# Performance work log

Measured on AMD Instinct MI355X. Metric: run time of the kernel, lower is better.

## Reference

```python
import jax, jax.numpy as jnp
import numpy as np

D_MODEL = 1024
DK = 64
H = D_MODEL // DK
EPS = 1e-5


def setup_inputs() -> dict:
    key = jax.random.key(0)
    ks = jax.random.split(key, 8)
    B, M = 4, 2048
    s = 1.0 / np.sqrt(D_MODEL)
    return {
        "inp": jax.random.normal(ks[0], (B, M, D_MODEL), dtype=jnp.float32),
        "Wq": jax.random.normal(ks[1], (D_MODEL, D_MODEL), dtype=jnp.float32) * s,
        "bq": jnp.zeros((D_MODEL,), dtype=jnp.float32),
        "Wk": jax.random.normal(ks[2], (D_MODEL, D_MODEL), dtype=jnp.float32) * s,
        "bk": jnp.zeros((D_MODEL,), dtype=jnp.float32),
        "Wv": jax.random.normal(ks[3], (D_MODEL, D_MODEL), dtype=jnp.float32) * s,
        "bv": jnp.zeros((D_MODEL,), dtype=jnp.float32),
        "gamma": jnp.ones((D_MODEL,), dtype=jnp.float32),
        "beta": jnp.zeros((D_MODEL,), dtype=jnp.float32),
    }


def reference(inp, Wq, bq, Wk, bk, Wv, bv, gamma, beta):
    B, M, _ = inp.shape
    # LayerNorm over last dim
    mu = jnp.mean(inp, axis=-1, keepdims=True)
    var = jnp.mean(jnp.square(inp - mu), axis=-1, keepdims=True)
    out = (inp - mu) * jax.lax.rsqrt(var + EPS) * gamma + beta
    # QKV projections (x @ W + b)
    Q = (out @ Wq + bq).reshape(B, M, DK, H)
    K = (out @ Wk + bk).reshape(B, M, DK, H)
    V = (out @ Wv + bv).reshape(B, M, DK, H)
    # per-position attention over the dk axis, contracting h
    scores = jnp.einsum("bmih,bmjh->bmij", Q, K) / np.sqrt(DK)  # [B,M,dk,dk]
    att = jax.nn.softmax(scores, axis=-1)
    res = jnp.einsum("bmij,bmjh->bmih", att, V).reshape(B, M, D_MODEL)
    # dropout is identity at eval; positionals add in original is dead code
    return inp + res
```

## Files before the change

### kernel.cpp

```cpp
#include <hip/hip_runtime.h>
#include <hip/hip_bf16.h>

#define D_MODEL 1024
#define NQKV 3072

typedef __attribute__((ext_vector_type(8))) short bf16x8;
typedef __attribute__((ext_vector_type(4))) float f32x4;
typedef __attribute__((ext_vector_type(16))) float f32x16;
typedef __attribute__((ext_vector_type(8))) unsigned short u16x8;

static __device__ __forceinline__ unsigned short f2bf(float f){
  unsigned int x = __float_as_uint(f);
  x += 0x7fff + ((x >> 16) & 1);
  return (unsigned short)(x >> 16);
}
static __device__ __forceinline__ float bf2f(unsigned short u){
  return __uint_as_float(((unsigned int)u) << 16);
}

__global__ __launch_bounds__(256) void ln_kernel(const float* __restrict__ inp,
    const float* __restrict__ gamma, const float* __restrict__ beta,
    unsigned short* __restrict__ X){
  const int row = blockIdx.x;
  const int t = threadIdx.x;
  const float4* ip = (const float4*)(inp + (size_t)row * D_MODEL);
  float4 v = ip[t];
  float s1 = v.x + v.y + v.z + v.w;
  float s2 = v.x*v.x + v.y*v.y + v.z*v.z + v.w*v.w;
#pragma unroll
  for (int off = 32; off >= 1; off >>= 1){
    s1 += __shfl_down(s1, off);
    s2 += __shfl_down(s2, off);
  }
  __shared__ float red[8];
  const int wave = t >> 6, lane = t & 63;
  if (lane == 0){ red[wave] = s1; red[4 + wave] = s2; }
  __syncthreads();
  s1 = red[0] + red[1] + red[2] + red[3];
  s2 = red[4] + red[5] + red[6] + red[7];
  const float mu   = s1 * (1.0f / D_MODEL);
  const float var  = s2 * (1.0f / D_MODEL) - mu * mu;
  const float rstd = rsqrtf(var + 1e-5f);
  float4 g = ((const float4*)gamma)[t];
  float4 b = ((const float4*)beta)[t];
  ushort4 o;
  o.x = f2bf((v.x - mu) * rstd * g.x + b.x);
  o.y = f2bf((v.y - mu) * rstd * g.y + b.y);
  o.z = f2bf((v.z - mu) * rstd * g.z + b.z);
  o.w = f2bf((v.w - mu) * rstd * g.w + b.w);
  ((ushort4*)(X + (size_t)row * D_MODEL))[t] = o;
}

__global__ __launch_bounds__(256) void wtrans_kernel(const float* __restrict__ Wq,
    const float* __restrict__ Wk, const float* __restrict__ Wv,
    const float* __restrict__ bq, const float* __restrict__ bk,
    const float* __restrict__ bv, unsigned short* __restrict__ Wt,
    float* __restrict__ bc){
  __shared__ float tile[32][33];
  const int z = blockIdx.z;
  const float* W = (z == 0) ? Wq : ((z == 1) ? Wk : Wv);
  const int k0 = blockIdx.x * 32, n0 = blockIdx.y * 32;
  const int r = threadIdx.x >> 5, c = threadIdx.x & 31;
  if (blockIdx.x == 0 && r == 0){
    const float* bsrc = (z == 0) ? bq : ((z == 1) ? bk : bv);
    bc[z * 1024 + n0 + c] = bsrc[n0 + c];
  }
#pragma unroll
  for (int i = 0; i < 4; i++)
    tile[r + i*8][c] = W[(size_t)(k0 + r + i*8) * D_MODEL + n0 + c];
  __syncthreads();
  unsigned short* dst = Wt + (size_t)(z * D_MODEL + n0) * D_MODEL + k0;
#pragma unroll
  for (int i = 0; i < 4; i++){
    int rr = r + i*8;
    dst[(size_t)rr * D_MODEL + c] = f2bf(tile[c][rr]);
  }
}


#define GLL(src, dst) __builtin_amdgcn_global_load_lds( \
    (const __attribute__((address_space(1))) void*)(src), \
    (__attribute__((address_space(3))) void*)(dst), 16, 0, 0)

#define STAGE(tsrc, bi) do { \
  _Pragma("unroll") \
  for (int q = 0; q < 4; q++){ \
    const int idx = q*512 + tid; \
    const int row = idx >> 3; \
    const size_t scol = (size_t)((tsrc)*128) + (((idx & 7)*16) ^ ((row & 7) << 4)); \
    GLL(Ag + (size_t)row*2048 + scol, ldsS + (size_t)(bi)*65536 + idx*16); \
    GLL(Bg + (size_t)row*2048 + scol, ldsS + (size_t)(bi)*65536 + 32768 + idx*16); \
  } \
} while(0)

#define BODY(bi) do { \
  const char* Ab = ldsS + (size_t)(bi)*65536 + (wr*128 + lr)*128; \
  const char* Bb = ldsS + (size_t)(bi)*65536 + 32768 + (wc*64 + lr)*128; \
  _Pragma("unroll") \
  for (int kh = 0; kh < 2; kh++){ \
    const int cb = kh ? colb1 : colb0; \
    bf16x8 Ar[8], Br[4]; \
    _Pragma("unroll") \
    for (int m = 0; m < 8; m++) Ar[m] = *(const bf16x8*)(Ab + m*2048 + cb); \
    _Pragma("unroll") \
    for (int n = 0; n < 4; n++) Br[n] = *(const bf16x8*)(Bb + n*2048 + cb); \
    _Pragma("unroll") \
    for (int m = 0; m < 8; m++) \
      _Pragma("unroll") \
      for (int n = 0; n < 4; n++) \
        acc[m][n] = __builtin_amdgcn_mfma_f32_16x16x32_bf16(Ar[m], Br[n], acc[m][n], 0, 0, 0); \
  } \
} while(0)

#define BARRIER __builtin_amdgcn_s_barrier()
#define SCHEDB  __builtin_amdgcn_sched_barrier(0)
#define VMCNT0  asm volatile("s_waitcnt vmcnt(0)" ::: "memory")

__global__ __launch_bounds__(512, 2) void gemm256_kernel(const unsigned short* __restrict__ A,
    const unsigned short* __restrict__ Bt, const float* __restrict__ bias,
    unsigned short* __restrict__ C){
  __shared__ __align__(16) char ldsS[2 * 65536];
  const int tid = threadIdx.x;
  const int wave = tid >> 6, lane = tid & 63;
  const int wr = wave >> 2, wc = wave & 3;
  const int lr = lane & 15;
  const int x7 = (lane & 7) << 4;
  const int colb0 = ((lane >> 4) * 16) ^ x7;
  const int colb1 = (64 + (lane >> 4) * 16) ^ x7;

  const int b = blockIdx.x;
  const int swz = (b & 7) * 48 + (b >> 3);
  const int m0 = (swz & 31) * 256;
  const int n0 = (swz >> 5) * 256;

  const char* Ag = (const char*)(A + (size_t)m0 * 1024);
  const char* Bg = (const char*)(Bt + (size_t)n0 * 1024);

  f32x4 acc[8][4] = {};

  STAGE(0, 0);
  SCHEDB; VMCNT0; BARRIER; SCHEDB;

  int buf = 0;
  for (int t = 0; t < 16; ++t, buf ^= 1){
    if (t < 15) STAGE(t + 1, buf ^ 1);
    BODY(buf);
    if (t < 15) { SCHEDB; VMCNT0; BARRIER; SCHEDB; }
  }

  const int gm = m0 + wr*128;
  const int gn = n0 + wc*64;
  const int rr0 = (lane >> 4) * 4;
#pragma unroll
  for (int nf = 0; nf < 4; nf++){
    const int gcol = gn + nf*16 + lr;
    const float bb = bias[gcol];
#pragma unroll
    for (int mf = 0; mf < 8; mf++){
      const int grow = gm + mf*16 + rr0;
#pragma unroll
      for (int r = 0; r < 4; r++)
        C[(size_t)(grow + r) * NQKV + gcol] = f2bf(acc[mf][nf][r] + bb);
    }
  }
}

__global__ __launch_bounds__(256) void attn_kernel(const unsigned short* __restrict__ qkv,
    const float* __restrict__ inp, float* __restrict__ out){
  __shared__ unsigned short P[4][64 * 64];
  const int wave = threadIdx.x >> 6, lane = threadIdx.x & 63;
  const int token = blockIdx.x * 4 + wave;
  const unsigned short* row = qkv + (size_t)token * NQKV;
  const int l31 = lane & 31, hi = lane >> 5;
  const int l15 = lane & 15, qg = lane >> 4;
  char* pbase = (char*)&P[wave][0];

  bf16x8 kf[2], qf[2];
#pragma unroll
  for (int mt = 0; mt < 2; mt++)
    kf[mt] = *(const bf16x8*)(row + 1024 + (mt*32 + l31)*16 + hi*8);
#pragma unroll
  for (int nt = 0; nt < 2; nt++)
    qf[nt] = *(const bf16x8*)(row + (nt*32 + l31)*16 + hi*8);

  bf16x8 vf[2];
#pragma unroll
  for (int kc = 0; kc < 2; kc++)
#pragma unroll
    for (int e = 0; e < 8; e++)
      vf[kc][e] = (short)row[2048 + (kc*32 + qg*8 + e)*16 + l15];

  f32x16 s[2][2] = {};
#pragma unroll
  for (int mt = 0; mt < 2; mt++)
#pragma unroll
    for (int nt = 0; nt < 2; nt++)
      s[mt][nt] = __builtin_amdgcn_mfma_f32_32x32x16_bf16(kf[mt], qf[nt], s[mt][nt], 0, 0, 0);

#pragma unroll
  for (int ti = 0; ti < 2; ti++){
    float m = s[0][ti][0];
#pragma unroll
    for (int mt = 0; mt < 2; mt++)
#pragma unroll
      for (int r = 0; r < 16; r++) m = fmaxf(m, s[mt][ti][r]);
    m = fmaxf(m, __shfl_xor(m, 32));
    float sum = 0.0f;
#pragma unroll
    for (int mt = 0; mt < 2; mt++)
#pragma unroll
      for (int r = 0; r < 16; r++){
        float p = exp2f((s[mt][ti][r] - m) * 0.1803368801f);
        s[mt][ti][r] = p;
        sum += p;
      }
    sum += __shfl_xor(sum, 32);
    const float invs = 1.0f / sum;
    const int i = ti*32 + l31;
    const int sw = (i & 7) << 4;
#pragma unroll
    for (int mt = 0; mt < 2; mt++)
#pragma unroll
      for (int g = 0; g < 4; g++){
        ushort4 pk;
        pk.x = f2bf(s[mt][ti][4*g + 0] * invs);
        pk.y = f2bf(s[mt][ti][4*g + 1] * invs);
        pk.z = f2bf(s[mt][ti][4*g + 2] * invs);
        pk.w = f2bf(s[mt][ti][4*g + 3] * invs);
        const int jbyte = mt*64 + g*16 + hi*8;
        *(ushort4*)(pbase + ((i*128 + jbyte) ^ sw)) = pk;
      }
  }
  __syncthreads();

  f32x4 o[4] = {};
#pragma unroll
  for (int nt = 0; nt < 4; nt++){
    const int n = nt*16 + l15;
    const int swr = (n & 7) << 4;
#pragma unroll
    for (int kc = 0; kc < 2; kc++){
      bf16x8 pb = *(const bf16x8*)(pbase + ((n*128 + kc*64 + qg*16) ^ swr));
      o[nt] = __builtin_amdgcn_mfma_f32_16x16x32_bf16(vf[kc], pb, o[nt], 0, 0, 0);
    }
  }

  const size_t base = (size_t)token * D_MODEL;
#pragma unroll
  for (int nt = 0; nt < 4; nt++){
    const int i = nt*16 + l15;
    const float4 iv = *(const float4*)(inp + base + i*16 + qg*4);
    float4 ov;
    ov.x = iv.x + o[nt][0];
    ov.y = iv.y + o[nt][1];
    ov.z = iv.z + o[nt][2];
    ov.w = iv.w + o[nt][3];
    *(float4*)(out + base + i*16 + qg*4) = ov;
  }
}

extern "C" void kernel_launch(void* const* d_in, const int* in_sizes, int n_in,
                              void* d_out, int out_size, void* d_ws, size_t ws_size,
                              hipStream_t stream) {
  const float* inp   = (const float*)d_in[0];
  const float* Wq    = (const float*)d_in[1];
  const float* bq    = (const float*)d_in[2];
  const float* Wk    = (const float*)d_in[3];
  const float* bk    = (const float*)d_in[4];
  const float* Wv    = (const float*)d_in[5];
  const float* bv    = (const float*)d_in[6];
  const float* gamma = (const float*)d_in[7];
  const float* beta  = (const float*)d_in[8];
  float* out = (float*)d_out;

  char* ws = (char*)d_ws;
  unsigned short* Xln  = (unsigned short*)ws;
  unsigned short* Wt   = (unsigned short*)(ws + 16777216);
  float*          bc   = (float*)(ws + 23068672);
  unsigned short* QKV  = (unsigned short*)(ws + 23080960);

  ln_kernel<<<8192, 256, 0, stream>>>(inp, gamma, beta, Xln);
  wtrans_kernel<<<dim3(32, 32, 3), 256, 0, stream>>>(Wq, Wk, Wv, bq, bk, bv, Wt, bc);
  gemm256_kernel<<<384, 512, 0, stream>>>(Xln, Wt, bc, QKV);
  attn_kernel<<<2048, 256, 0, stream>>>(QKV, inp, out);
}
```

Before: 105.1 us.

## Restructure QKV GEMM into per-wave private LDS staging with 128x256 tiles

```diff
diff --git a/kernel.cpp b/kernel.cpp
--- a/kernel.cpp
+++ b/kernel.cpp
@@ -82,81 +82,79 @@
     (const __attribute__((address_space(1))) void*)(src), \
     (__attribute__((address_space(3))) void*)(dst), 16, 0, 0)
 
-#define STAGE(tsrc, bi) do { \
-  _Pragma("unroll") \
-  for (int q = 0; q < 4; q++){ \
-    const int idx = q*512 + tid; \
-    const int row = idx >> 3; \
-    const size_t scol = (size_t)((tsrc)*128) + (((idx & 7)*16) ^ ((row & 7) << 4)); \
-    GLL(Ag + (size_t)row*2048 + scol, ldsS + (size_t)(bi)*65536 + idx*16); \
-    GLL(Bg + (size_t)row*2048 + scol, ldsS + (size_t)(bi)*65536 + 32768 + idx*16); \
+#define STG(t, bi) do { \
+  _Pragma("unroll") \
+  for (int j = 0; j < 4; j++){ \
+    GLL(As + (size_t)j*32768 + (size_t)(t)*64, dstL + (bi)*8192 + j*1024); \
+    GLL(Bs + (size_t)j*32768 + (size_t)(t)*64, dstL + (bi)*8192 + 4096 + j*1024); \
   } \
 } while(0)
 
-#define BODY(bi) do { \
-  const char* Ab = ldsS + (size_t)(bi)*65536 + (wr*128 + lr)*128; \
-  const char* Bb = ldsS + (size_t)(bi)*65536 + 32768 + (wc*64 + lr)*128; \
-  _Pragma("unroll") \
-  for (int kh = 0; kh < 2; kh++){ \
-    const int cb = kh ? colb1 : colb0; \
-    bf16x8 Ar[8], Br[4]; \
+#define BDY(bi) do { \
+  const char* Ab = wlds + (bi)*8192 + fo; \
+  const char* Bb = Ab + 4096; \
+  bf16x8 Af[4], Bf[4]; \
+  _Pragma("unroll") \
+  for (int m = 0; m < 4; m++) Af[m] = *(const bf16x8*)(Ab + m*1024); \
+  _Pragma("unroll") \
+  for (int n = 0; n < 4; n++) Bf[n] = *(const bf16x8*)(Bb + n*1024); \
+  _Pragma("unroll") \
+  for (int m = 0; m < 4; m++) \
     _Pragma("unroll") \
-    for (int m = 0; m < 8; m++) Ar[m] = *(const bf16x8*)(Ab + m*2048 + cb); \
-    _Pragma("unroll") \
-    for (int n = 0; n < 4; n++) Br[n] = *(const bf16x8*)(Bb + n*2048 + cb); \
-    _Pragma("unroll") \
-    for (int m = 0; m < 8; m++) \
-      _Pragma("unroll") \
-      for (int n = 0; n < 4; n++) \
-        acc[m][n] = __builtin_amdgcn_mfma_f32_16x16x32_bf16(Ar[m], Br[n], acc[m][n], 0, 0, 0); \
-  } \
+    for (int n = 0; n < 4; n++) \
+      acc[m][n] = __builtin_amdgcn_mfma_f32_16x16x32_bf16(Af[m], Bf[n], acc[m][n], 0, 0, 0); \
 } while(0)
 
-#define BARRIER __builtin_amdgcn_s_barrier()
 #define SCHEDB  __builtin_amdgcn_sched_barrier(0)
+#define VMCNT8  asm volatile("s_waitcnt vmcnt(8)" ::: "memory")
 #define VMCNT0  asm volatile("s_waitcnt vmcnt(0)" ::: "memory")
-
-__global__ __launch_bounds__(512, 2) void gemm256_kernel(const unsigned short* __restrict__ A,
+#define LGKM0   asm volatile("s_waitcnt lgkmcnt(0)" ::: "memory")
+
+__global__ __launch_bounds__(512, 2) void gemm_pw_kernel(const unsigned short* __restrict__ A,
     const unsigned short* __restrict__ Bt, const float* __restrict__ bias,
     unsigned short* __restrict__ C){
-  __shared__ __align__(16) char ldsS[2 * 65536];
+  __shared__ __align__(16) char ldsS[131072];
   const int tid = threadIdx.x;
   const int wave = tid >> 6, lane = tid & 63;
   const int wr = wave >> 2, wc = wave & 3;
-  const int lr = lane & 15;
-  const int x7 = (lane & 7) << 4;
-  const int colb0 = ((lane >> 4) * 16) ^ x7;
-  const int colb1 = (64 + (lane >> 4) * 16) ^ x7;
 
   const int b = blockIdx.x;
-  const int swz = (b & 7) * 48 + (b >> 3);
-  const int m0 = (swz & 31) * 256;
-  const int n0 = (swz >> 5) * 256;
-
-  const char* Ag = (const char*)(A + (size_t)m0 * 1024);
-  const char* Bg = (const char*)(Bt + (size_t)n0 * 1024);
-
-  f32x4 acc[8][4] = {};
-
-  STAGE(0, 0);
-  SCHEDB; VMCNT0; BARRIER; SCHEDB;
-
+  const int swz = (b & 7) * 96 + (b >> 3);
+  const int m0 = (swz & 63) * 128;
+  const int n0 = (swz >> 6) * 256;
+
+  const int r0l = ((lane & 32) >> 2) + (lane & 7);
+  const int kgl = (lane >> 3) & 3;
+  const char* As = (const char*)(A  + (size_t)(m0 + wr*64 + r0l) * 1024) + kgl*16;
+  const char* Bs = (const char*)(Bt + (size_t)(n0 + wc*64 + r0l) * 1024) + kgl*16;
+  char* wlds = ldsS + wave*16384;
+  char* dstL = wlds + lane*16;
+
+  const int lr = lane & 15, kgr = lane >> 4;
+  const int fo = (((lr & 8) << 2) | (kgr << 3) | (lr & 7)) << 4;
+
+  f32x4 acc[4][4] = {};
+
+  STG(0, 0);
   int buf = 0;
-  for (int t = 0; t < 16; ++t, buf ^= 1){
-    if (t < 15) STAGE(t + 1, buf ^ 1);
-    BODY(buf);
-    if (t < 15) { SCHEDB; VMCNT0; BARRIER; SCHEDB; }
-  }
-
-  const int gm = m0 + wr*128;
+  for (int t = 0; t < 31; ++t, buf ^= 1){
+    SCHEDB; LGKM0; SCHEDB;
+    STG(t + 1, buf ^ 1);
+    VMCNT8; SCHEDB;
+    BDY(buf);
+  }
+  SCHEDB; VMCNT0; SCHEDB;
+  BDY(buf);
+
+  const int gm = m0 + wr*64;
   const int gn = n0 + wc*64;
-  const int rr0 = (lane >> 4) * 4;
+  const int rr0 = kgr * 4;
 #pragma unroll
   for (int nf = 0; nf < 4; nf++){
     const int gcol = gn + nf*16 + lr;
     const float bb = bias[gcol];
 #pragma unroll
-    for (int mf = 0; mf < 8; mf++){
+    for (int mf = 0; mf < 4; mf++){
       const int grow = gm + mf*16 + rr0;
 #pragma unroll
       for (int r = 0; r < 4; r++)
@@ -281,6 +279,6 @@
 
   ln_kernel<<<8192, 256, 0, stream>>>(inp, gamma, beta, Xln);
   wtrans_kernel<<<dim3(32, 32, 3), 256, 0, stream>>>(Wq, Wk, Wv, bq, bk, bv, Wt, bc);
-  gemm256_kernel<<<384, 512, 0, stream>>>(Xln, Wt, bc, QKV);
+  gemm_pw_kernel<<<768, 512, 0, stream>>>(Xln, Wt, bc, QKV);
   attn_kernel<<<2048, 256, 0, stream>>>(QKV, inp, out);
 }
```

Result: slower. 214.6 us (+104.1%).
